# Kernel optimization log

Measured on AMD Instinct MI355X. Metric: run time of the kernel, lower is better.

The kernel has to match this reference:

```python
import jax, jax.numpy as jnp
import numpy as np

B, M, N, DQ, H = 4, 4096, 4096, 256, 64

def setup_inputs() -> dict:
    key = jax.random.key(0)
    k1, k2, k3, k4 = jax.random.split(key, 4)
    x = jax.random.normal(k1, (B, M, DQ), dtype=jnp.float32)
    cond = jax.random.normal(k2, (B, N, DQ), dtype=jnp.float32)
    Wq = jax.random.normal(k3, (DQ, H), dtype=jnp.float32) * (1.0 / np.sqrt(DQ))
    Wkv = jax.random.normal(k4, (DQ, 2 * H), dtype=jnp.float32) * (1.0 / np.sqrt(DQ))
    return {"x": x, "cond": cond, "Wq": Wq, "Wkv": Wkv}

def reference(x, cond, Wq, Wkv):
    h = Wq.shape[1]
    q = jnp.einsum('bmi,ih->bmh', x, Wq)          # [B,M,H]
    kv = jnp.einsum('bni,ih->bnh', cond, Wkv)     # [B,N,2H]
    k, v = jnp.split(kv, 2, axis=-1)              # each [B,N,H]
    qk = jnp.einsum('bmd,bnd->bmn', q, k) / jnp.sqrt(jnp.asarray(h, q.dtype))
    attn = jax.nn.softmax(qk, axis=-1)            # [B,M,N]
    out = jnp.einsum('bmn,bnd->bmd', attn, v)     # [B,M,H]
    return out
```

## Files before the change

### kernel.cpp

```cpp
#include <hip/hip_runtime.h>
#include <hip/hip_bf16.h>
#include <cstdint>


#define BB 4
#define MM 4096
#define NN 4096
#define DQm 256
#define DH 64
#define NSP 4
#define QSCALE 0.18033688011112042f

typedef _Float16 half8 __attribute__((ext_vector_type(8)));
typedef _Float16 half4 __attribute__((ext_vector_type(4)));
typedef float floatx16 __attribute__((ext_vector_type(16)));

static __device__ __forceinline__ unsigned pkrtz(float a, float b) {
    union { __fp16 h __attribute__((ext_vector_type(2))); unsigned u; } cv;
    cv.h = __builtin_amdgcn_cvt_pkrtz(a, b);
    return cv.u;
}

__global__ __launch_bounds__(256) void wtrans_kernel(const float* __restrict__ Wq,
                                                     const float* __restrict__ Wkv,
                                                     _Float16* __restrict__ wt) {
    int cout = blockIdx.x;
    int t = threadIdx.x;
    float v = (cout < 64) ? Wq[t * 64 + cout] * QSCALE : Wkv[t * 128 + (cout - 64)];
    _Float16 hi = (_Float16)v;
    _Float16 lo = (_Float16)(v - (float)hi);
    wt[cout * DQm + t] = hi;
    wt[192 * DQm + cout * DQm + t] = lo;
}

__global__ __launch_bounds__(256) void qproj_kernel(const float* __restrict__ x,
                                                    const _Float16* __restrict__ wt,
                                                    _Float16* __restrict__ q_h) {
    __shared__ __align__(16) _Float16 xh[64][264];
    __shared__ __align__(16) _Float16 xl[64][264];
    const int t = threadIdx.x;
    const long row0 = (long)blockIdx.x * 64;
    const float4* xg = (const float4*)(x + row0 * DQm);
#pragma unroll
    for (int it = 0; it < 16; ++it) {
        int fid = t + it * 256;
        int row = fid >> 6, c4 = fid & 63;
        float4 v = xg[fid];
        half4 hh = {(_Float16)v.x, (_Float16)v.y, (_Float16)v.z, (_Float16)v.w};
        half4 hl = {(_Float16)(v.x - (float)hh[0]), (_Float16)(v.y - (float)hh[1]),
                    (_Float16)(v.z - (float)hh[2]), (_Float16)(v.w - (float)hh[3])};
        *(half4*)(&xh[row][c4 * 4]) = hh;
        *(half4*)(&xl[row][c4 * 4]) = hl;
    }
    __syncthreads();
    const int lane = t & 63, w = t >> 6, c = lane & 31, h = lane >> 5;
    const int rt = w & 1, ct = w >> 1;
    const _Float16* wlo = wt + 192 * DQm;
    floatx16 a1, a2, a3;
#pragma unroll
    for (int i = 0; i < 16; ++i) { a1[i] = 0.f; a2[i] = 0.f; a3[i] = 0.f; }
#pragma unroll
    for (int kt = 0; kt < 16; ++kt) {
        half8 ah = *(const half8*)(&xh[rt * 32 + c][kt * 16 + h * 8]);
        half8 al = *(const half8*)(&xl[rt * 32 + c][kt * 16 + h * 8]);
        half8 bh = *(const half8*)(wt  + (long)(ct * 32 + c) * DQm + kt * 16 + h * 8);
        half8 bl = *(const half8*)(wlo + (long)(ct * 32 + c) * DQm + kt * 16 + h * 8);
        a1 = __builtin_amdgcn_mfma_f32_32x32x16_f16(ah, bh, a1, 0, 0, 0);
        a2 = __builtin_amdgcn_mfma_f32_32x32x16_f16(ah, bl, a2, 0, 0, 0);
        a3 = __builtin_amdgcn_mfma_f32_32x32x16_f16(al, bh, a3, 0, 0, 0);
    }
#pragma unroll
    for (int r = 0; r < 16; ++r) {
        int m = (r & 3) + 8 * (r >> 2) + 4 * h;
        q_h[(row0 + rt * 32 + m) * DH + ct * 32 + c] = (_Float16)(a1[r] + a2[r] + a3[r]);
    }
}

__global__ __launch_bounds__(256) void kvproj_kernel(const float* __restrict__ cond,
                                                     const _Float16* __restrict__ wt,
                                                     _Float16* __restrict__ k_h,
                                                     _Float16* __restrict__ vt_h) {
    __shared__ __align__(16) _Float16 xh[64][264];
    __shared__ __align__(16) _Float16 xl[64][264];
    const int t = threadIdx.x;
    const long row0 = (long)blockIdx.x * 64;
    const float4* xg = (const float4*)(cond + row0 * DQm);
#pragma unroll
    for (int it = 0; it < 16; ++it) {
        int fid = t + it * 256;
        int row = fid >> 6, c4 = fid & 63;
        float4 v = xg[fid];
        half4 hh = {(_Float16)v.x, (_Float16)v.y, (_Float16)v.z, (_Float16)v.w};
        half4 hl = {(_Float16)(v.x - (float)hh[0]), (_Float16)(v.y - (float)hh[1]),
                    (_Float16)(v.z - (float)hh[2]), (_Float16)(v.w - (float)hh[3])};
        *(half4*)(&xh[row][c4 * 4]) = hh;
        *(half4*)(&xl[row][c4 * 4]) = hl;
    }
    __syncthreads();
    const int lane = t & 63, w = t >> 6, c = lane & 31, h = lane >> 5;
    const int rt = w & 1, ctp = w >> 1;
    const _Float16* wlo = wt + 192 * DQm;
    floatx16 a1[2], a2[2], a3[2];
#pragma unroll
    for (int i = 0; i < 16; ++i) {
        a1[0][i] = 0.f; a2[0][i] = 0.f; a3[0][i] = 0.f;
        a1[1][i] = 0.f; a2[1][i] = 0.f; a3[1][i] = 0.f;
    }
#pragma unroll
    for (int kt = 0; kt < 16; ++kt) {
        half8 ah = *(const half8*)(&xh[rt * 32 + c][kt * 16 + h * 8]);
        half8 al = *(const half8*)(&xl[rt * 32 + c][kt * 16 + h * 8]);
#pragma unroll
        for (int i = 0; i < 2; ++i) {
            long wrow = 64 + (ctp * 2 + i) * 32 + c;
            half8 bh = *(const half8*)(wt  + wrow * DQm + kt * 16 + h * 8);
            half8 bl = *(const half8*)(wlo + wrow * DQm + kt * 16 + h * 8);
            a1[i] = __builtin_amdgcn_mfma_f32_32x32x16_f16(ah, bh, a1[i], 0, 0, 0);
            a2[i] = __builtin_amdgcn_mfma_f32_32x32x16_f16(ah, bl, a2[i], 0, 0, 0);
            a3[i] = __builtin_amdgcn_mfma_f32_32x32x16_f16(al, bh, a3[i], 0, 0, 0);
        }
    }
#pragma unroll
    for (int i = 0; i < 2; ++i) {
        int cout = (ctp * 2 + i) * 32 + c;
        if (cout < 64) {
#pragma unroll
            for (int r = 0; r < 16; ++r) {
                int m = (r & 3) + 8 * (r >> 2) + 4 * h;
                k_h[(row0 + rt * 32 + m) * DH + cout] =
                    (_Float16)(a1[i][r] + a2[i][r] + a3[i][r]);
            }
        } else {
            int d = cout - 64;
            long bb = row0 >> 12;
#pragma unroll
            for (int s2 = 0; s2 < 4; ++s2) {
                long n = row0 + rt * 32 + 8 * s2 + 4 * h;
                half4 hv;
#pragma unroll
                for (int j = 0; j < 4; ++j)
                    hv[j] = (_Float16)(a1[i][s2 * 4 + j] + a2[i][s2 * 4 + j] +
                                       a3[i][s2 * 4 + j]);
                *(half4*)(vt_h + (bb * DH + d) * NN + (n & 4095)) = hv;
            }
        }
    }
}

__global__ __launch_bounds__(256, 2) void fa_kernel(const _Float16* __restrict__ q_h,
                                                    const _Float16* __restrict__ k_h,
                                                    const _Float16* __restrict__ vt_h,
                                                    float* __restrict__ Opart,
                                                    float2* __restrict__ ml) {
    __shared__ __align__(16) _Float16 k_lds[64][72];
    __shared__ __align__(16) _Float16 vt_lds[64][72];

    const int t = threadIdx.x;
    const int w = t >> 6;
    const int lane = t & 63;
    const int c = lane & 31;
    const int h = lane >> 5;

    const int bid = blockIdx.x;
    const int sp = bid >> 7;
    const int b  = (bid >> 5) & 3;
    const int mt = bid & 31;
    const int mbase = mt * 128 + w * 32;
    const long qrow = (long)b * MM + mbase + c;

    half8 qf[4];
#pragma unroll
    for (int kt = 0; kt < 4; ++kt)
        qf[kt] = *(const half8*)(q_h + qrow * DH + kt * 16 + h * 8);

    floatx16 Oc0, Oc1;
#pragma unroll
    for (int i = 0; i < 16; ++i) { Oc0[i] = 0.f; Oc1[i] = 0.f; }
    float m_run = -INFINITY, l_run = 0.f;

#pragma unroll 1
    for (int nt = sp * 16; nt < sp * 16 + 16; ++nt) {
        const int n0 = nt * 64;
        __syncthreads();
        {
            const uint4* kg = (const uint4*)(k_h + ((long)b * NN + n0) * DH);
#pragma unroll
            for (int it = 0; it < 2; ++it) {
                int cid = t + it * 256;
                int r = cid >> 3, q = cid & 7;
                *(uint4*)(&k_lds[r][q * 8]) = kg[cid];
                *(uint4*)(&vt_lds[r][q * 8]) =
                    *(const uint4*)(vt_h + ((long)b * DH + r) * NN + n0 + q * 8);
            }
        }
        __syncthreads();

        floatx16 Sc[2];
#pragma unroll
        for (int a = 0; a < 2; ++a) {
            floatx16 acc;
#pragma unroll
            for (int i = 0; i < 16; ++i) acc[i] = 0.f;
#pragma unroll
            for (int kt = 0; kt < 4; ++kt) {
                half8 af = *(const half8*)(&k_lds[a * 32 + c][kt * 16 + h * 8]);
                acc = __builtin_amdgcn_mfma_f32_32x32x16_f16(af, qf[kt], acc, 0, 0, 0);
            }
            Sc[a] = acc;
        }

        float tmax = -INFINITY;
#pragma unroll
        for (int a = 0; a < 2; ++a)
#pragma unroll
            for (int r = 0; r < 16; ++r) tmax = fmaxf(tmax, Sc[a][r]);
        tmax = fmaxf(tmax, __shfl_xor(tmax, 32, 64));
        float m_new = fmaxf(m_run, tmax);
        float alpha = exp2f(m_run - m_new);
        float tsum = 0.f;
#pragma unroll
        for (int a = 0; a < 2; ++a)
#pragma unroll
            for (int r = 0; r < 16; ++r) {
                float p = exp2f(Sc[a][r] - m_new);
                Sc[a][r] = p;
                tsum += p;
            }
        tsum += __shfl_xor(tsum, 32, 64);
        l_run = l_run * alpha + tsum;
        m_run = m_new;
#pragma unroll
        for (int i = 0; i < 16; ++i) { Oc0[i] *= alpha; Oc1[i] *= alpha; }

#pragma unroll
        for (int a = 0; a < 2; ++a) {
            uint2 pk0 = {pkrtz(Sc[a][0],  Sc[a][1]),  pkrtz(Sc[a][2],  Sc[a][3])};
            uint2 pk1 = {pkrtz(Sc[a][4],  Sc[a][5]),  pkrtz(Sc[a][6],  Sc[a][7])};
            uint2 pk2 = {pkrtz(Sc[a][8],  Sc[a][9]),  pkrtz(Sc[a][10], Sc[a][11])};
            uint2 pk3 = {pkrtz(Sc[a][12], Sc[a][13]), pkrtz(Sc[a][14], Sc[a][15])};
            uint2 s0, s1, ex0, ex1;
            s0.x = h ? pk0.x : pk1.x;  s0.y = h ? pk0.y : pk1.y;
            s1.x = h ? pk2.x : pk3.x;  s1.y = h ? pk2.y : pk3.y;
            ex0.x = __shfl_xor((int)s0.x, 32, 64);
            ex0.y = __shfl_xor((int)s0.y, 32, 64);
            ex1.x = __shfl_xor((int)s1.x, 32, 64);
            ex1.y = __shfl_xor((int)s1.y, 32, 64);
            union { uint4 u; half8 f; } f0, f1;
            f0.u.x = h ? ex0.x : pk0.x;  f0.u.y = h ? ex0.y : pk0.y;
            f0.u.z = h ? pk1.x : ex0.x;  f0.u.w = h ? pk1.y : ex0.y;
            f1.u.x = h ? ex1.x : pk2.x;  f1.u.y = h ? ex1.y : pk2.y;
            f1.u.z = h ? pk3.x : ex1.x;  f1.u.w = h ? pk3.y : ex1.y;
#pragma unroll
            for (int bq = 0; bq < 2; ++bq) {
                int kt = 2 * a + bq;
                half8 pf = bq ? f1.f : f0.f;
                half8 vf0 = *(const half8*)(&vt_lds[c][kt * 16 + h * 8]);
                half8 vf1 = *(const half8*)(&vt_lds[32 + c][kt * 16 + h * 8]);
                Oc0 = __builtin_amdgcn_mfma_f32_32x32x16_f16(vf0, pf, Oc0, 0, 0, 0);
                Oc1 = __builtin_amdgcn_mfma_f32_32x32x16_f16(vf1, pf, Oc1, 0, 0, 0);
            }
        }
    }

    const long obase = ((long)sp * BB * MM + (long)b * MM + mbase + c) * DH;
#pragma unroll
    for (int dt = 0; dt < 2; ++dt) {
        const floatx16& O = dt ? Oc1 : Oc0;
#pragma unroll
        for (int s2 = 0; s2 < 4; ++s2) {
            float4 v;
            v.x = O[s2 * 4 + 0]; v.y = O[s2 * 4 + 1];
            v.z = O[s2 * 4 + 2]; v.w = O[s2 * 4 + 3];
            *(float4*)(Opart + obase + dt * 32 + s2 * 8 + h * 4) = v;
        }
    }
    if (h == 0)
        ml[((long)sp * BB + b) * MM + mbase + c] = make_float2(m_run, l_run);
}

__global__ __launch_bounds__(256) void merge_kernel(const float* __restrict__ Opart,
                                                    const float2* __restrict__ ml,
                                                    float* __restrict__ out) {
    const long gid = (long)blockIdx.x * 256 + threadIdx.x;
    const long row = gid >> 6;
    float2 p[NSP];
    float mmax = -INFINITY;
#pragma unroll
    for (int i = 0; i < NSP; ++i) {
        p[i] = ml[(long)i * BB * MM + row];
        mmax = fmaxf(mmax, p[i].x);
    }
    float denom = 0.f, o = 0.f;
#pragma unroll
    for (int i = 0; i < NSP; ++i) {
        float ai = exp2f(p[i].x - mmax);
        denom += ai * p[i].y;
        o += ai * Opart[(long)i * BB * MM * DH + gid];
    }
    out[gid] = o / denom;
}

extern "C" void kernel_launch(void* const* d_in, const int* in_sizes, int n_in,
                              void* d_out, int out_size, void* d_ws, size_t ws_size,
                              hipStream_t stream) {
    const float* x    = (const float*)d_in[0];
    const float* cond = (const float*)d_in[1];
    const float* Wq   = (const float*)d_in[2];
    const float* Wkv  = (const float*)d_in[3];
    float* out = (float*)d_out;

    char* ws = (char*)d_ws;
    _Float16* wt   = (_Float16*)(ws);
    _Float16* q_h  = (_Float16*)(ws + 196608);
    _Float16* k_h  = (_Float16*)(ws + 196608 + 2097152);
    _Float16* vt_h = (_Float16*)(ws + 196608 + 2 * 2097152);
    float*    Op   = (float*)(ws + 196608 + 3 * 2097152);
    float2*   mlp  = (float2*)(ws + 196608 + 3 * 2097152 + (size_t)NSP * 4194304);

    wtrans_kernel<<<192, 256, 0, stream>>>(Wq, Wkv, wt);
    qproj_kernel<<<BB * MM / 64, 256, 0, stream>>>(x, wt, q_h);
    kvproj_kernel<<<BB * NN / 64, 256, 0, stream>>>(cond, wt, k_h, vt_h);
    fa_kernel<<<NSP * BB * 32, 256, 0, stream>>>(q_h, k_h, vt_h, Op, mlp);
    merge_kernel<<<BB * MM * DH / 256, 256, 0, stream>>>(Op, mlp, out);
}
```

Before: 137.9 us.

## Fuse projections into one LDS-free kernel, prefetch K/V tiles, vectorize merge

Merges the Q and KV projection kernels into one launch in which each wave computes a 32x32 output tile, reading fp32 rows straight from global memory and splitting them to fp16 hi/lo in registers instead of staging through LDS. The attention kernel now software-prefetches the next K/V tile into registers while the current tile is computed, hiding global load latency behind the MFMA work. The merge kernel processes four outputs per thread with float4 loads and stores. The trade-off is that the fused projection drops cross-wave reuse of the A rows through LDS, so it does more redundant global reads, and the prefetch raises register pressure in the attention kernel.

After: 143.0 us. +3.8%, slower.

```diff
diff --git a/kernel.cpp b/kernel.cpp
--- a/kernel.cpp
+++ b/kernel.cpp
@@ -33,114 +33,72 @@
     wt[192 * DQm + cout * DQm + t] = lo;
 }
 
-__global__ __launch_bounds__(256) void qproj_kernel(const float* __restrict__ x,
-                                                    const _Float16* __restrict__ wt,
-                                                    _Float16* __restrict__ q_h) {
-    __shared__ __align__(16) _Float16 xh[64][264];
-    __shared__ __align__(16) _Float16 xl[64][264];
+__global__ __launch_bounds__(256, 3) void proj_kernel(const float* __restrict__ x,
+                                                      const float* __restrict__ cond,
+                                                      const _Float16* __restrict__ wt,
+                                                      _Float16* __restrict__ q_h,
+                                                      _Float16* __restrict__ k_h,
+                                                      _Float16* __restrict__ vt_h) {
     const int t = threadIdx.x;
-    const long row0 = (long)blockIdx.x * 64;
-    const float4* xg = (const float4*)(x + row0 * DQm);
-#pragma unroll
-    for (int it = 0; it < 16; ++it) {
-        int fid = t + it * 256;
-        int row = fid >> 6, c4 = fid & 63;
-        float4 v = xg[fid];
-        half4 hh = {(_Float16)v.x, (_Float16)v.y, (_Float16)v.z, (_Float16)v.w};
-        half4 hl = {(_Float16)(v.x - (float)hh[0]), (_Float16)(v.y - (float)hh[1]),
-                    (_Float16)(v.z - (float)hh[2]), (_Float16)(v.w - (float)hh[3])};
-        *(half4*)(&xh[row][c4 * 4]) = hh;
-        *(half4*)(&xl[row][c4 * 4]) = hl;
-    }
-    __syncthreads();
-    const int lane = t & 63, w = t >> 6, c = lane & 31, h = lane >> 5;
-    const int rt = w & 1, ct = w >> 1;
-    const _Float16* wlo = wt + 192 * DQm;
+    const int w = t >> 6, lane = t & 63, c = lane & 31, h = lane >> 5;
+    const int W = blockIdx.x * 4 + w;
+    const bool isq = W < 1024;
+    int rowtile, colbase;
+    const float* src;
+    if (isq) { rowtile = W >> 1; colbase = (W & 1) * 32; src = x; }
+    else { int W2 = W - 1024; rowtile = W2 >> 2; colbase = (W2 & 3) * 32; src = cond; }
+    const long rowbase = (long)rowtile * 32;
+    const float* arow = src + (rowbase + c) * DQm;
+    const _Float16* bh_p = wt + (long)((isq ? 0 : 64) + colbase + c) * DQm;
+    const _Float16* bl_p = bh_p + 192 * DQm;
+
     floatx16 a1, a2, a3;
 #pragma unroll
     for (int i = 0; i < 16; ++i) { a1[i] = 0.f; a2[i] = 0.f; a3[i] = 0.f; }
 #pragma unroll
     for (int kt = 0; kt < 16; ++kt) {
-        half8 ah = *(const half8*)(&xh[rt * 32 + c][kt * 16 + h * 8]);
-        half8 al = *(const half8*)(&xl[rt * 32 + c][kt * 16 + h * 8]);
-        half8 bh = *(const half8*)(wt  + (long)(ct * 32 + c) * DQm + kt * 16 + h * 8);
-        half8 bl = *(const half8*)(wlo + (long)(ct * 32 + c) * DQm + kt * 16 + h * 8);
+        const int off = kt * 16 + h * 8;
+        float4 v0 = *(const float4*)(arow + off);
+        float4 v1 = *(const float4*)(arow + off + 4);
+        half8 ah = {(_Float16)v0.x, (_Float16)v0.y, (_Float16)v0.z, (_Float16)v0.w,
+                    (_Float16)v1.x, (_Float16)v1.y, (_Float16)v1.z, (_Float16)v1.w};
+        half8 al = {(_Float16)(v0.x - (float)ah[0]), (_Float16)(v0.y - (float)ah[1]),
+                    (_Float16)(v0.z - (float)ah[2]), (_Float16)(v0.w - (float)ah[3]),
+                    (_Float16)(v1.x - (float)ah[4]), (_Float16)(v1.y - (float)ah[5]),
+                    (_Float16)(v1.z - (float)ah[6]), (_Float16)(v1.w - (float)ah[7])};
+        half8 bh = *(const half8*)(bh_p + off);
+        half8 bl = *(const half8*)(bl_p + off);
         a1 = __builtin_amdgcn_mfma_f32_32x32x16_f16(ah, bh, a1, 0, 0, 0);
         a2 = __builtin_amdgcn_mfma_f32_32x32x16_f16(ah, bl, a2, 0, 0, 0);
         a3 = __builtin_amdgcn_mfma_f32_32x32x16_f16(al, bh, a3, 0, 0, 0);
     }
-#pragma unroll
-    for (int r = 0; r < 16; ++r) {
-        int m = (r & 3) + 8 * (r >> 2) + 4 * h;
-        q_h[(row0 + rt * 32 + m) * DH + ct * 32 + c] = (_Float16)(a1[r] + a2[r] + a3[r]);
-    }
-}
-
-__global__ __launch_bounds__(256) void kvproj_kernel(const float* __restrict__ cond,
-                                                     const _Float16* __restrict__ wt,
-                                                     _Float16* __restrict__ k_h,
-                                                     _Float16* __restrict__ vt_h) {
-    __shared__ __align__(16) _Float16 xh[64][264];
-    __shared__ __align__(16) _Float16 xl[64][264];
-    const int t = threadIdx.x;
-    const long row0 = (long)blockIdx.x * 64;
-    const float4* xg = (const float4*)(cond + row0 * DQm);
-#pragma unroll
-    for (int it = 0; it < 16; ++it) {
-        int fid = t + it * 256;
-        int row = fid >> 6, c4 = fid & 63;
-        float4 v = xg[fid];
-        half4 hh = {(_Float16)v.x, (_Float16)v.y, (_Float16)v.z, (_Float16)v.w};
-        half4 hl = {(_Float16)(v.x - (float)hh[0]), (_Float16)(v.y - (float)hh[1]),
-                    (_Float16)(v.z - (float)hh[2]), (_Float16)(v.w - (float)hh[3])};
-        *(half4*)(&xh[row][c4 * 4]) = hh;
-        *(half4*)(&xl[row][c4 * 4]) = hl;
-    }
-    __syncthreads();
-    const int lane = t & 63, w = t >> 6, c = lane & 31, h = lane >> 5;
-    const int rt = w & 1, ctp = w >> 1;
-    const _Float16* wlo = wt + 192 * DQm;
-    floatx16 a1[2], a2[2], a3[2];
-#pragma unroll
-    for (int i = 0; i < 16; ++i) {
-        a1[0][i] = 0.f; a2[0][i] = 0.f; a3[0][i] = 0.f;
-        a1[1][i] = 0.f; a2[1][i] = 0.f; a3[1][i] = 0.f;
-    }
-#pragma unroll
-    for (int kt = 0; kt < 16; ++kt) {
-        half8 ah = *(const half8*)(&xh[rt * 32 + c][kt * 16 + h * 8]);
-        half8 al = *(const half8*)(&xl[rt * 32 + c][kt * 16 + h * 8]);
-#pragma unroll
-        for (int i = 0; i < 2; ++i) {
-            long wrow = 64 + (ctp * 2 + i) * 32 + c;
-            half8 bh = *(const half8*)(wt  + wrow * DQm + kt * 16 + h * 8);
-            half8 bl = *(const half8*)(wlo + wrow * DQm + kt * 16 + h * 8);
-            a1[i] = __builtin_amdgcn_mfma_f32_32x32x16_f16(ah, bh, a1[i], 0, 0, 0);
-            a2[i] = __builtin_amdgcn_mfma_f32_32x32x16_f16(ah, bl, a2[i], 0, 0, 0);
-            a3[i] = __builtin_amdgcn_mfma_f32_32x32x16_f16(al, bh, a3[i], 0, 0, 0);
-        }
-    }
-#pragma unroll
-    for (int i = 0; i < 2; ++i) {
-        int cout = (ctp * 2 + i) * 32 + c;
+
+    if (isq) {
+#pragma unroll
+        for (int r = 0; r < 16; ++r) {
+            int m = (r & 3) + 8 * (r >> 2) + 4 * h;
+            q_h[(rowbase + m) * DH + colbase + c] =
+                (_Float16)(a1[r] + a2[r] + a3[r]);
+        }
+    } else {
+        int cout = colbase + c;
         if (cout < 64) {
 #pragma unroll
             for (int r = 0; r < 16; ++r) {
                 int m = (r & 3) + 8 * (r >> 2) + 4 * h;
-                k_h[(row0 + rt * 32 + m) * DH + cout] =
-                    (_Float16)(a1[i][r] + a2[i][r] + a3[i][r]);
+                k_h[(rowbase + m) * DH + cout] =
+                    (_Float16)(a1[r] + a2[r] + a3[r]);
             }
         } else {
             int d = cout - 64;
-            long bb = row0 >> 12;
+            long bb = rowbase >> 12;
 #pragma unroll
             for (int s2 = 0; s2 < 4; ++s2) {
-                long n = row0 + rt * 32 + 8 * s2 + 4 * h;
+                long n = rowbase + 8 * s2 + 4 * h;
                 half4 hv;
 #pragma unroll
                 for (int j = 0; j < 4; ++j)
-                    hv[j] = (_Float16)(a1[i][s2 * 4 + j] + a2[i][s2 * 4 + j] +
-                                       a3[i][s2 * 4 + j]);
+                    hv[j] = (_Float16)(a1[s2 * 4 + j] + a2[s2 * 4 + j] + a3[s2 * 4 + j]);
                 *(half4*)(vt_h + (bb * DH + d) * NN + (n & 4095)) = hv;
             }
         }
@@ -173,25 +131,31 @@
     for (int kt = 0; kt < 4; ++kt)
         qf[kt] = *(const half8*)(q_h + qrow * DH + kt * 16 + h * 8);
 
+    const uint4* kp = (const uint4*)(k_h + ((long)b * NN + sp * 16 * 64) * DH) + t;
+    const _Float16* vbase =
+        vt_h + ((long)b * DH + (t >> 3)) * NN + sp * 16 * 64 + (t & 7) * 8;
+    const uint4* vp0 = (const uint4*)vbase;
+    const uint4* vp1 = (const uint4*)(vbase + 32 * NN);
+
+    uint4 kr0 = kp[0], kr1 = kp[256];
+    uint4 vr0 = *vp0, vr1 = *vp1;
+
     floatx16 Oc0, Oc1;
 #pragma unroll
     for (int i = 0; i < 16; ++i) { Oc0[i] = 0.f; Oc1[i] = 0.f; }
     float m_run = -INFINITY, l_run = 0.f;
 
 #pragma unroll 1
-    for (int nt = sp * 16; nt < sp * 16 + 16; ++nt) {
-        const int n0 = nt * 64;
+    for (int it = 0; it < 16; ++it) {
         __syncthreads();
-        {
-            const uint4* kg = (const uint4*)(k_h + ((long)b * NN + n0) * DH);
-#pragma unroll
-            for (int it = 0; it < 2; ++it) {
-                int cid = t + it * 256;
-                int r = cid >> 3, q = cid & 7;
-                *(uint4*)(&k_lds[r][q * 8]) = kg[cid];
-                *(uint4*)(&vt_lds[r][q * 8]) =
-                    *(const uint4*)(vt_h + ((long)b * DH + r) * NN + n0 + q * 8);
-            }
+        *(uint4*)(&k_lds[t >> 3][(t & 7) * 8]) = kr0;
+        *(uint4*)(&k_lds[32 + (t >> 3)][(t & 7) * 8]) = kr1;
+        *(uint4*)(&vt_lds[t >> 3][(t & 7) * 8]) = vr0;
+        *(uint4*)(&vt_lds[32 + (t >> 3)][(t & 7) * 8]) = vr1;
+        kp += 512; vp0 += 8; vp1 += 8;
+        if (it < 15) {
+            kr0 = kp[0]; kr1 = kp[256];
+            vr0 = *vp0;  vr1 = *vp1;
         }
         __syncthreads();
 
@@ -282,7 +246,7 @@
                                                     const float2* __restrict__ ml,
                                                     float* __restrict__ out) {
     const long gid = (long)blockIdx.x * 256 + threadIdx.x;
-    const long row = gid >> 6;
+    const long row = gid >> 4;
     float2 p[NSP];
     float mmax = -INFINITY;
 #pragma unroll
@@ -290,14 +254,18 @@
         p[i] = ml[(long)i * BB * MM + row];
         mmax = fmaxf(mmax, p[i].x);
     }
-    float denom = 0.f, o = 0.f;
+    float denom = 0.f;
+    float4 o = {0.f, 0.f, 0.f, 0.f};
 #pragma unroll
     for (int i = 0; i < NSP; ++i) {
         float ai = exp2f(p[i].x - mmax);
         denom += ai * p[i].y;
-        o += ai * Opart[(long)i * BB * MM * DH + gid];
-    }
-    out[gid] = o / denom;
+        float4 v = *(const float4*)(Opart + ((long)i * BB * MM * DH) + gid * 4);
+        o.x += ai * v.x; o.y += ai * v.y; o.z += ai * v.z; o.w += ai * v.w;
+    }
+    float inv = 1.f / denom;
+    o.x *= inv; o.y *= inv; o.z *= inv; o.w *= inv;
+    *(float4*)(out + gid * 4) = o;
 }
 
 extern "C" void kernel_launch(void* const* d_in, const int* in_sizes, int n_in,
@@ -318,8 +286,7 @@
     float2*   mlp  = (float2*)(ws + 196608 + 3 * 2097152 + (size_t)NSP * 4194304);
 
     wtrans_kernel<<<192, 256, 0, stream>>>(Wq, Wkv, wt);
-    qproj_kernel<<<BB * MM / 64, 256, 0, stream>>>(x, wt, q_h);
-    kvproj_kernel<<<BB * NN / 64, 256, 0, stream>>>(cond, wt, k_h, vt_h);
+    proj_kernel<<<768, 256, 0, stream>>>(x, cond, wt, q_h, k_h, vt_h);
     fa_kernel<<<NSP * BB * 32, 256, 0, stream>>>(q_h, k_h, vt_h, Op, mlp);
-    merge_kernel<<<BB * MM * DH / 256, 256, 0, stream>>>(Op, mlp, out);
-}
+    merge_kernel<<<BB * MM * DH / 1024, 256, 0, stream>>>(Op, mlp, out);
+}
```
